# Optimization experiments

Measured on AMD Instinct MI355X. Metric: run time of the kernel, lower is better.

Reference implementation:

```python
import jax, jax.numpy as jnp
import numpy as np

N_NODES = 50000
N_EDGES = 800000
D_IN = 64
D_OUT = 64
N_REL = 8


def setup_inputs() -> dict:
    key = jax.random.key(0)
    ks = jax.random.split(key, 7)
    x = jax.random.normal(ks[0], (N_NODES, D_IN), jnp.float32)
    src = jax.random.randint(ks[1], (N_EDGES,), 0, N_NODES)   # neighbor ids
    dst = jax.random.randint(ks[2], (N_EDGES,), 0, N_NODES)   # center node ids
    rel = jax.random.randint(ks[3], (N_EDGES,), 0, N_REL)
    # xavier_uniform for W_r: [R, 2*d, d]
    lim = float(np.sqrt(6.0 / (2 * D_IN + D_IN)))
    W_r = jax.random.uniform(ks[4], (N_REL, 2 * D_IN, D_IN), jnp.float32, -lim, lim)
    # nn.Linear(2*d, d_out): weight [d_out, 2*d], bias [d_out]
    lim2 = float(1.0 / np.sqrt(2 * D_IN))
    W_lin = jax.random.uniform(ks[5], (D_OUT, 2 * D_IN), jnp.float32, -lim2, lim2)
    b_lin = jax.random.uniform(ks[6], (D_OUT,), jnp.float32, -lim2, lim2)
    return {"x": x, "src": src, "dst": dst, "rel": rel,
            "W_r": W_r, "W_lin": W_lin, "b_lin": b_lin}


def reference(x, src, dst, rel, W_r, W_lin, b_lin):
    n, d = x.shape
    e = src.shape[0]
    # gate logit per edge: (concat(x[dst], x[src]) @ W_r[rel]).sum(-1)
    # == concat(x[dst], x[src]) . W_r[rel].sum(-1)  -- mathematically identical,
    # avoids materializing the [E, 2d, d] matmul the torch loop performs.
    w = W_r.sum(-1)                      # [R, 2d]
    w_dst, w_src = w[:, :d], w[:, d:]    # [R, d] each
    logit = jnp.sum(x[dst] * w_dst[rel], axis=-1) + jnp.sum(x[src] * w_src[rel], axis=-1)  # [E]
    gate = jax.nn.sigmoid(logit)[:, None]        # [E, 1]
    weighted = x[src] * gate                     # [E, d]
    # scatter-mean over destination nodes (nodes with no edges stay zero)
    agg_sum = jax.ops.segment_sum(weighted, dst, num_segments=n)            # [N, d]
    cnt = jax.ops.segment_sum(jnp.ones((e,), x.dtype), dst, num_segments=n)  # [N]
    agg = agg_sum / jnp.maximum(cnt, 1.0)[:, None]
    combined = jnp.concatenate([x, agg], axis=-1)  # [N, 2d]
    out = combined @ W_lin.T + b_lin               # [N, d_out]
    return jax.nn.leaky_relu(out, negative_slope=0.01)
```

## Files before the change

### kernel.cpp

```cpp
#include <hip/hip_runtime.h>
#include <hip/hip_fp16.h>
#include <cmath>

#define N_NODES 50000
#define N_EDGES 800000
#define D 64
#define N_REL 8

#define NODES_PER_BLK 32
#define TN 16
#define MAXDEG 64

typedef __attribute__((ext_vector_type(8))) short bf16x8;
typedef __attribute__((ext_vector_type(4))) float f32x4;
union FragU { uint4 u; bf16x8 b; };

static __device__ __forceinline__ unsigned f2bf(float f) {
    unsigned u = __float_as_uint(f);
    return (u + 0x7FFFu + ((u >> 16) & 1u)) >> 16;
}
#define BFLO(u) __uint_as_float((u) << 16)
#define BFHI(u) __uint_as_float((u) & 0xFFFF0000u)

__global__ void wprep_kernel(const float* __restrict__ W_r, float* __restrict__ w,
                             int* __restrict__ cnt) {
    int t = blockIdx.x * blockDim.x + threadIdx.x;
    if (t < N_REL * 2 * D) {
        const float* p = W_r + (size_t)t * D;
        float s = 0.0f;
#pragma unroll
        for (int k = 0; k < D; ++k) s += p[k];
        w[t] = s;
    }
    for (int i = t; i < N_NODES; i += gridDim.x * blockDim.x)
        cnt[i] = 0;
}

__global__ __launch_bounds__(256) void tables_kernel(
    const float* __restrict__ x, const float* __restrict__ w,
    float* __restrict__ Dn, float* __restrict__ Sr,
    unsigned short* __restrict__ xb)
{
    __shared__ float xs[TN][68];
    __shared__ float ws[16][68];

    int tid = threadIdx.x;
    int n0  = blockIdx.x * TN;

    for (int i = tid; i < 16 * 64; i += 256)
        ws[i >> 6][i & 63] = w[i];
    for (int i = tid; i < TN * 64; i += 256) {
        int n = n0 + (i >> 6);
        xs[i >> 6][i & 63] = (n < N_NODES) ? x[(size_t)n * D + (i & 63)] : 0.f;
    }
    __syncthreads();

    for (int i = tid; i < TN * 64; i += 256) {
        int n = n0 + (i >> 6);
        if (n < N_NODES) xb[(size_t)n0 * D + i] = (unsigned short)f2bf(xs[i >> 6][i & 63]);
    }

    int q = tid & 15, nl = tid >> 4;
    float acc = 0.f;
#pragma unroll
    for (int k = 0; k < 64; k += 4) {
        float4 a = *(const float4*)&xs[nl][k];
        float4 b = *(const float4*)&ws[q][k];
        acc += a.x * b.x + a.y * b.y + a.z * b.z + a.w * b.w;
    }
    int n = n0 + nl;
    if (n < N_NODES) {
        int r = q >> 1;
        if ((q & 1) == 0) Dn[n * 8 + r] = acc;
        else              Sr[n * 8 + r] = acc;
    }
}

__global__ __launch_bounds__(256) void scatter_kernel(
    const int* __restrict__ src, const int* __restrict__ dst,
    const int* __restrict__ rel,
    int* __restrict__ cnt,
    const float* __restrict__ Dn, const float* __restrict__ Sr,
    unsigned int* __restrict__ epack) {
    int e = blockIdx.x * 256 + threadIdx.x;

    int d = dst[e];
    int s = src[e];
    int r = rel[e];

    int rank = atomicAdd(&cnt[d], 1);

    float logit = Dn[d * 8 + r] + Sr[s * 8 + r];
    float gate = 1.0f / (1.0f + __expf(-logit));
    if (rank < MAXDEG) {
        unsigned pv = ((unsigned)__half_as_ushort(__float2half_rn(gate)) << 16)
                    | (unsigned)s;
        epack[(size_t)d * MAXDEG + rank] = pv;
    }
}

__global__ __launch_bounds__(256) void agglin_kernel(
    const unsigned short* __restrict__ xb,
    const unsigned int* __restrict__ xbu,
    const int*   __restrict__ cnt,
    const unsigned int* __restrict__ epack,
    const float* __restrict__ W_lin,
    const float* __restrict__ b_lin,
    float* __restrict__ out)
{
    __shared__ unsigned int W2[64][68];
    __shared__ unsigned int c2[NODES_PER_BLK][68];
    __shared__ float b_lds[64];

    int tid  = threadIdx.x;
    int n0   = blockIdx.x * NODES_PER_BLK;
    int lane = tid & 63;
    int wv   = tid >> 6;

    for (int i = tid; i < 64 * 64; i += 256) {
        int j = i >> 6, kp = i & 63;
        float2 wvv = *(const float2*)&W_lin[j * 128 + kp * 2];
        W2[j][kp] = f2bf(wvv.x) | (f2bf(wvv.y) << 16);
    }
    if (tid < 64) b_lds[tid] = b_lin[tid];

    for (int i = tid; i < NODES_PER_BLK * 32; i += 256) {
        int nl = i >> 5, kp = i & 31;
        int n  = n0 + nl;
        c2[nl][kp] = (n < N_NODES) ? xbu[(size_t)n * 32 + kp] : 0u;
    }

    int nbase = n0 + wv * 8;

    int      degv[8];
    unsigned ev[8];
#pragma unroll
    for (int i = 0; i < 8; ++i) {
        int n = nbase + i;
        degv[i] = (n < N_NODES) ? cnt[n] : 0;
    }
#pragma unroll
    for (int i = 0; i < 8; ++i) {
        int n = nbase + i;
        ev[i] = (n < N_NODES) ? epack[(size_t)n * MAXDEG + lane] : 0u;
    }

    int sub = lane >> 4;
    int q   = lane & 15;
    int q4  = q * 4;

#pragma unroll
    for (int i = 0; i < 8; ++i) {
        int m = (degv[i] < MAXDEG) ? degv[i] : MAXDEG;
        unsigned e_m = (lane < m) ? ev[i] : 0u;
        float gl = __half2float(__ushort_as_half((unsigned short)(e_m >> 16)));
        int   ol = (int)(e_m & 0xFFFFu) * D;

        float ax = 0.f, ay = 0.f, az = 0.f, aw = 0.f;
        for (int base = 0; base < m; base += 8) {
            int e0 = base + sub;
            int e1 = base + 4 + sub;
            float g0 = __shfl(gl, e0, 64);
            int   o0 = __shfl(ol, e0, 64);
            float g1 = __shfl(gl, e1, 64);
            int   o1 = __shfl(ol, e1, 64);
            uint2 u0 = *(const uint2*)&xb[(size_t)o0 + q4];
            uint2 u1 = *(const uint2*)&xb[(size_t)o1 + q4];
            ax += g0 * BFLO(u0.x) + g1 * BFLO(u1.x);
            ay += g0 * BFHI(u0.x) + g1 * BFHI(u1.x);
            az += g0 * BFLO(u0.y) + g1 * BFLO(u1.y);
            aw += g0 * BFHI(u0.y) + g1 * BFHI(u1.y);
        }

#pragma unroll
        for (int off = 16; off <= 32; off <<= 1) {
            ax += __shfl_xor(ax, off, 64);
            ay += __shfl_xor(ay, off, 64);
            az += __shfl_xor(az, off, 64);
            aw += __shfl_xor(aw, off, 64);
        }

        if (sub == 0) {
            float inv = 1.0f / fmaxf((float)degv[i], 1.0f);
            int nl = wv * 8 + i;
            c2[nl][32 + 2 * q]     = f2bf(ax * inv) | (f2bf(ay * inv) << 16);
            c2[nl][32 + 2 * q + 1] = f2bf(az * inv) | (f2bf(aw * inv) << 16);
        }
    }
    __syncthreads();

    int mtile = wv & 1;
    int nt0   = wv >> 1;
    int lrow  = lane & 15;
    int kgrp  = lane >> 4;

    float bias0 = b_lds[nt0 * 16 + lrow];
    float bias1 = b_lds[(nt0 + 2) * 16 + lrow];
    f32x4 acc0 = {bias0, bias0, bias0, bias0};
    f32x4 acc1 = {bias1, bias1, bias1, bias1};

#pragma unroll
    for (int ks = 0; ks < 4; ++ks) {
        int cb = ks * 16 + kgrp * 4;
        FragU a, b0, b1;
        a.u  = *(const uint4*)&c2[mtile * 16 + lrow][cb];
        b0.u = *(const uint4*)&W2[nt0 * 16 + lrow][cb];
        b1.u = *(const uint4*)&W2[(nt0 + 2) * 16 + lrow][cb];
        acc0 = __builtin_amdgcn_mfma_f32_16x16x32_bf16(a.b, b0.b, acc0, 0, 0, 0);
        acc1 = __builtin_amdgcn_mfma_f32_16x16x32_bf16(a.b, b1.b, acc1, 0, 0, 0);
    }

#pragma unroll
    for (int i = 0; i < 4; ++i) {
        int node = n0 + mtile * 16 + kgrp * 4 + i;
        if (node < N_NODES) {
            float v0 = acc0[i]; v0 = (v0 > 0.f) ? v0 : 0.01f * v0;
            float v1 = acc1[i]; v1 = (v1 > 0.f) ? v1 : 0.01f * v1;
            out[(size_t)node * D + nt0 * 16 + lrow]       = v0;
            out[(size_t)node * D + (nt0 + 2) * 16 + lrow] = v1;
        }
    }
}

extern "C" void kernel_launch(void* const* d_in, const int* in_sizes, int n_in,
                              void* d_out, int out_size, void* d_ws, size_t ws_size,
                              hipStream_t stream) {
    const float* x     = (const float*)d_in[0];
    const int*   src   = (const int*)  d_in[1];
    const int*   dst   = (const int*)  d_in[2];
    const int*   rel   = (const int*)  d_in[3];
    const float* W_r   = (const float*)d_in[4];
    const float* W_lin = (const float*)d_in[5];
    const float* b_lin = (const float*)d_in[6];
    float* out = (float*)d_out;

    char* p = (char*)d_ws;
    float*  w       = (float*)p;                p += 4096;
    float*  Dn      = (float*)p;                p += (size_t)N_NODES * 8 * 4;
    float*  Sr      = (float*)p;                p += (size_t)N_NODES * 8 * 4;
    int*    cnt     = (int*)p;                  p += 256 * 1024;
    unsigned int* epack = (unsigned int*)p;     p += (size_t)N_NODES * MAXDEG * 4;
    unsigned short* xb = (unsigned short*)p;    p += (size_t)N_NODES * D * 2;

    wprep_kernel<<<512, 256, 0, stream>>>(W_r, w, cnt);
    tables_kernel<<<(N_NODES + TN - 1) / TN, 256, 0, stream>>>(x, w, Dn, Sr, xb);
    scatter_kernel<<<N_EDGES / 256, 256, 0, stream>>>(
        src, dst, rel, cnt, Dn, Sr, epack);
    agglin_kernel<<<(N_NODES + NODES_PER_BLK - 1) / NODES_PER_BLK, 256, 0, stream>>>(
        xb, (const unsigned int*)xb, cnt, epack, W_lin, b_lin, out);
}
```

Before: 169.0 us.

## Partition scatter by destination segment and interleave gathers across nodes

The scatter kernel now launches 8x as many blocks. Each block reads its edge chunk but handles only edges whose destination falls in its 6250-node segment, with blockIdx mod 8 selecting the segment. Adjacent blocks therefore hit one segment of the cnt/epack arrays, which is meant to localise atomics and stores in L2/MALL, at the cost of reading the edge arrays 8 times. The aggregation loop is also restructured to walk all 8 nodes per wave together up to the maximum degree. This gives more independent gathers in flight but uses more registers and does wasted iterations for low-degree nodes.

```diff
diff --git a/kernel.cpp b/kernel.cpp
--- a/kernel.cpp
+++ b/kernel.cpp
@@ -10,6 +10,8 @@
 #define NODES_PER_BLK 32
 #define TN 16
 #define MAXDEG 64
+#define NSEG 8
+#define SEG_DIV 6250
 
 typedef __attribute__((ext_vector_type(8))) short bf16x8;
 typedef __attribute__((ext_vector_type(4))) float f32x4;
@@ -82,11 +84,17 @@
     int* __restrict__ cnt,
     const float* __restrict__ Dn, const float* __restrict__ Sr,
     unsigned int* __restrict__ epack) {
-    int e = blockIdx.x * 256 + threadIdx.x;
+    int seg   = blockIdx.x & (NSEG - 1);
+    int chunk = blockIdx.x >> 3;
+    int e = chunk * 256 + threadIdx.x;
+    if (e >= N_EDGES) return;
 
     int d = dst[e];
     int s = src[e];
     int r = rel[e];
+    asm volatile("" :: "v"(d), "v"(s), "v"(r));
+
+    if ((unsigned)d / SEG_DIV != (unsigned)seg) return;
 
     int rank = atomicAdd(&cnt[d], 1);
 
@@ -132,7 +140,7 @@
 
     int nbase = n0 + wv * 8;
 
-    int      degv[8];
+    int      degv[8], mm[8];
     unsigned ev[8];
 #pragma unroll
     for (int i = 0; i < 8; ++i) {
@@ -149,42 +157,51 @@
     int q   = lane & 15;
     int q4  = q * 4;
 
-#pragma unroll
-    for (int i = 0; i < 8; ++i) {
-        int m = (degv[i] < MAXDEG) ? degv[i] : MAXDEG;
-        unsigned e_m = (lane < m) ? ev[i] : 0u;
-        float gl = __half2float(__ushort_as_half((unsigned short)(e_m >> 16)));
-        int   ol = (int)(e_m & 0xFFFFu) * D;
-
-        float ax = 0.f, ay = 0.f, az = 0.f, aw = 0.f;
-        for (int base = 0; base < m; base += 8) {
-            int e0 = base + sub;
-            int e1 = base + 4 + sub;
-            float g0 = __shfl(gl, e0, 64);
-            int   o0 = __shfl(ol, e0, 64);
-            float g1 = __shfl(gl, e1, 64);
-            int   o1 = __shfl(ol, e1, 64);
+    int mmax = 0;
+    float gl[8]; int ol[8];
+#pragma unroll
+    for (int i = 0; i < 8; ++i) {
+        mm[i] = (degv[i] < MAXDEG) ? degv[i] : MAXDEG;
+        mmax  = (mm[i] > mmax) ? mm[i] : mmax;
+        unsigned e_m = (lane < mm[i]) ? ev[i] : 0u;
+        gl[i] = __half2float(__ushort_as_half((unsigned short)(e_m >> 16)));
+        ol[i] = (int)(e_m & 0xFFFFu) * D;
+    }
+
+    float ax[8], ay[8], az[8], aw[8];
+#pragma unroll
+    for (int i = 0; i < 8; ++i) { ax[i] = 0.f; ay[i] = 0.f; az[i] = 0.f; aw[i] = 0.f; }
+
+    for (int base = 0; base < mmax; base += 8) {
+#pragma unroll
+        for (int i = 0; i < 8; ++i) {
+            float g0 = __shfl(gl[i], base + sub, 64);
+            int   o0 = __shfl(ol[i], base + sub, 64);
+            float g1 = __shfl(gl[i], base + 4 + sub, 64);
+            int   o1 = __shfl(ol[i], base + 4 + sub, 64);
             uint2 u0 = *(const uint2*)&xb[(size_t)o0 + q4];
             uint2 u1 = *(const uint2*)&xb[(size_t)o1 + q4];
-            ax += g0 * BFLO(u0.x) + g1 * BFLO(u1.x);
-            ay += g0 * BFHI(u0.x) + g1 * BFHI(u1.x);
-            az += g0 * BFLO(u0.y) + g1 * BFLO(u1.y);
-            aw += g0 * BFHI(u0.y) + g1 * BFHI(u1.y);
-        }
-
+            ax[i] += g0 * BFLO(u0.x) + g1 * BFLO(u1.x);
+            ay[i] += g0 * BFHI(u0.x) + g1 * BFHI(u1.x);
+            az[i] += g0 * BFLO(u0.y) + g1 * BFLO(u1.y);
+            aw[i] += g0 * BFHI(u0.y) + g1 * BFHI(u1.y);
+        }
+    }
+
+#pragma unroll
+    for (int i = 0; i < 8; ++i) {
 #pragma unroll
         for (int off = 16; off <= 32; off <<= 1) {
-            ax += __shfl_xor(ax, off, 64);
-            ay += __shfl_xor(ay, off, 64);
-            az += __shfl_xor(az, off, 64);
-            aw += __shfl_xor(aw, off, 64);
-        }
-
+            ax[i] += __shfl_xor(ax[i], off, 64);
+            ay[i] += __shfl_xor(ay[i], off, 64);
+            az[i] += __shfl_xor(az[i], off, 64);
+            aw[i] += __shfl_xor(aw[i], off, 64);
+        }
         if (sub == 0) {
             float inv = 1.0f / fmaxf((float)degv[i], 1.0f);
             int nl = wv * 8 + i;
-            c2[nl][32 + 2 * q]     = f2bf(ax * inv) | (f2bf(ay * inv) << 16);
-            c2[nl][32 + 2 * q + 1] = f2bf(az * inv) | (f2bf(aw * inv) << 16);
+            c2[nl][32 + 2 * q]     = f2bf(ax[i] * inv) | (f2bf(ay[i] * inv) << 16);
+            c2[nl][32 + 2 * q + 1] = f2bf(az[i] * inv) | (f2bf(aw[i] * inv) << 16);
         }
     }
     __syncthreads();
@@ -244,7 +261,7 @@
 
     wprep_kernel<<<512, 256, 0, stream>>>(W_r, w, cnt);
     tables_kernel<<<(N_NODES + TN - 1) / TN, 256, 0, stream>>>(x, w, Dn, Sr, xb);
-    scatter_kernel<<<N_EDGES / 256, 256, 0, stream>>>(
+    scatter_kernel<<<NSEG * ((N_EDGES + 255) / 256), 256, 0, stream>>>(
         src, dst, rel, cnt, Dn, Sr, epack);
     agglin_kernel<<<(N_NODES + NODES_PER_BLK - 1) / NODES_PER_BLK, 256, 0, stream>>>(
         xb, (const unsigned int*)xb, cnt, epack, W_lin, b_lin, out);
```

Result: slower. 174.7 us (+3.4%).
